# Performance work log

Hardware: AMD Instinct MI355X
Metric: run time of the kernel (lower is better)

The kernel has to match this reference:

```python
import jax, jax.numpy as jnp
import numpy as np

HOP = 256
B, F, NB = 16, 4096, 65

def setup_inputs() -> dict:
    key = jax.random.key(0)
    k1, k2 = jax.random.split(key)
    filter_bank = jax.random.normal(k1, (B, F, NB), dtype=jnp.float32)
    noise_u = jax.random.uniform(k2, (B, F, HOP), dtype=jnp.float32)
    return {"filter_bank": filter_bank, "noise_u": noise_u}

def amp_to_impulse_response(amp, target_size):
    # treat real amp as complex spectrum with zero imag, go to time domain
    amp_c = jax.lax.complex(amp, jnp.zeros_like(amp))
    ir = jnp.fft.irfft(amp_c, axis=-1)            # [B, F, 2*(NB-1)]
    filter_size = ir.shape[-1]
    ir = jnp.roll(ir, filter_size // 2, axis=-1)
    n = jnp.arange(filter_size, dtype=ir.dtype)
    win = 0.5 * (1.0 - jnp.cos(2.0 * jnp.pi * n / filter_size))  # periodic hann (torch default)
    ir = ir * win
    ir = jnp.pad(ir, ((0, 0), (0, 0), (0, target_size - filter_size)))
    ir = jnp.roll(ir, -(filter_size // 2), axis=-1)
    return ir

def fft_convolve(signal, kernel):
    n = signal.shape[-1]
    sig = jnp.pad(signal, ((0, 0), (0, 0), (0, n)))
    ker = jnp.pad(kernel, ((0, 0), (0, 0), (kernel.shape[-1], 0)))
    out = jnp.fft.irfft(jnp.fft.rfft(sig) * jnp.fft.rfft(ker))
    return out[..., out.shape[-1] // 2:]

def reference(filter_bank, noise_u):
    impulse = amp_to_impulse_response(filter_bank, HOP)   # [B, F, HOP]
    noise = noise_u * 2.0 - 1.0                           # [B, F, HOP]
    out = fft_convolve(noise, impulse)                    # [B, F, HOP]
    return out.reshape(out.shape[0], -1, 1)               # [B, F*HOP, 1]
```

## Files before the change

### kernel.cpp

```cpp
#include <hip/hip_runtime.h>
#include <math.h>

#define NB 65
#define HOPS 256
#define RPB 4
#define THREADS 64
#define TAPS_OFF 360
#define RSTRIDE 492

#define PHYS(i) ((i) + (((i) >> 5) << 2))

#define WAVE_FENCE() do { asm volatile("" ::: "memory"); __builtin_amdgcn_wave_barrier(); } while (0)

__device__ __forceinline__ void load16(float (&d)[16], const float* p) {
#pragma unroll
    for (int x = 0; x < 4; ++x) {
        float4 v = *(const float4*)(p + 4 * x);
        d[4*x] = v.x; d[4*x+1] = v.y; d[4*x+2] = v.z; d[4*x+3] = v.w;
    }
}
__device__ __forceinline__ void load16s(float (&d)[16], const float* rowbuf, int L) {
#pragma unroll
    for (int x = 0; x < 4; ++x) {
        float4 v = *(const float4*)(rowbuf + PHYS(L + 4 * x));
        d[4*x] = v.x; d[4*x+1] = v.y; d[4*x+2] = v.z; d[4*x+3] = v.w;
    }
}
__device__ __forceinline__ void fma16(float (&f)[16], const float (&tp)[16],
                                      const float (&lo)[16], const float (&hi)[16]) {
#pragma unroll
    for (int kk = 0; kk < 16; ++kk) {
        float t = tp[kk];
#pragma unroll
        for (int d = 0; d < 16; ++d) {
            int j = 16 + d - kk;
            f[d] = fmaf(t, (j < 16) ? lo[j] : hi[j - 16], f[d]);
        }
    }
}

__global__ __launch_bounds__(THREADS, 4) void noisefilter_kernel(
    const float* __restrict__ fb,
    const float* __restrict__ nz,
    float* __restrict__ out)
{
    __shared__ float lds[RPB * RSTRIDE];
    const int tid  = threadIdx.x;
    const int lane = tid;
    const int r    = tid >> 4;
    const int l16  = tid & 15;
    const int t0   = l16 << 4;
    const size_t row0 = (size_t)blockIdx.x * RPB;
    float* rowbuf = &lds[r * RSTRIDE];

    {
        const float* fbw = fb + row0 * NB;
        for (int i = lane; i < RPB * NB; i += 64) {
            int rr = i / NB;
            int k  = i - rr * NB;
            lds[rr * RSTRIDE + TAPS_OFF + k] = fbw[i];
        }
    }

    const float4* nz4 = (const float4*)(nz + row0 * HOPS);
    float4 nv[4];
#pragma unroll
    for (int p = 0; p < 4; ++p) nv[p] = nz4[lane + p * 64];

    WAVE_FENCE();

    const float alphaA = (float)l16 * 0.04908738521234052f;
    const float alphaB = alphaA + 0.7853981633974483f;
    const float cA = __cosf(alphaA), cB = __cosf(alphaB);
    const float c2A = fmaf(2.0f * cA, cA, -1.0f);
    const float c2B = fmaf(2.0f * cB, cB, -1.0f);
    const float k2A = c2A + c2A, k2B = c2B + c2B;

    float eA1=0.f,eA2=0.f,oA1=0.f,oA2=0.f;
    float eB1=0.f,eB2=0.f,oB1=0.f,oB2=0.f;
    float s32 = 0.f, a0r = 0.f, a64r;

    const float* amp = rowbuf + TAPS_OFF;
    {
        float a = amp[64];
        a64r = a;
        { float t = a - eA2; float s = fmaf(k2A, eA1, t); eA2 = eA1; eA1 = s; }
        { float t = a - eB2; float s = fmaf(k2B, eB1, t); eB2 = eB1; eB1 = s; }
        s32 += a;
    }
#pragma unroll
    for (int kb = 48; kb >= 0; kb -= 16) {
        float ab[16];
        load16(ab, amp + kb);
#pragma unroll
        for (int kk = 15; kk >= 0; --kk) {
            float a = ab[kk];
            if (kk & 1) {
                { float t = a - oA2; float s = fmaf(k2A, oA1, t); oA2 = oA1; oA1 = s; }
                { float t = a - oB2; float s = fmaf(k2B, oB1, t); oB2 = oB1; oB1 = s; }
            } else {
                { float t = a - eA2; float s = fmaf(k2A, eA1, t); eA2 = eA1; eA1 = s; }
                { float t = a - eB2; float s = fmaf(k2B, eB1, t); eB2 = eB1; eB1 = s; }
                if ((kk >> 1) & 1) s32 -= a; else s32 += a;
            }
        }
        if (kb == 0) a0r = ab[0];
    }

    const float EA = fmaf(-c2A, eA2, eA1);
    const float OA = cA * (oA1 - oA2);
    const float EB = fmaf(-c2B, eB2, eB1);
    const float OB = cB * (oB1 - oB2);
    const float pm = (l16 & 1) ? -1.f : 1.f;
    const float corr = fmaf(pm, a64r, a0r);
    const float inv = 1.0f / 256.0f;
    float* tps = rowbuf + TAPS_OFF;

    {
        float GA  = fmaf(2.f, EA + OA, -corr);
        float GAm = fmaf(2.f, EA - OA, -corr);
        float TA  = GA  * (1.0f + cA) * inv;
        float TAm = GAm * (1.0f - cA) * inv;
        tps[l16] = TA;
        tps[64 - l16] = TAm;
        if (l16 >= 1) { tps[128 - l16] = TA; tps[64 + l16] = TAm; }
    }
    {
        float GB  = fmaf(2.f, EB + OB, -corr);
        float GBm = fmaf(2.f, EB - OB, -corr);
        float TB  = GB  * (1.0f + cB) * inv;
        float TBm = GBm * (1.0f - cB) * inv;
        tps[16 + l16] = TB;  tps[112 - l16] = TB;
        tps[48 - l16] = TBm; tps[80 + l16]  = TBm;
    }
    if (l16 == 0) {
        float G32 = fmaf(2.f, s32, -(a0r + a64r));
        float T32 = G32 * inv;
        tps[32] = T32;
        tps[96] = T32;
    }

    *(float4*)(rowbuf + PHYS(4 * l16)) = make_float4(0.f, 0.f, 0.f, 0.f);

#pragma unroll
    for (int p = 0; p < 4; ++p) {
        float4 v = nv[p];
        int o = (lane << 2) + 64;
        *(float4*)(&lds[p * RSTRIDE + PHYS(o)]) =
            make_float4(fmaf(2.f, v.x, -1.f), fmaf(2.f, v.y, -1.f),
                        fmaf(2.f, v.z, -1.f), fmaf(2.f, v.w, -1.f));
    }

    WAVE_FENCE();

    float f[16];
#pragma unroll
    for (int d = 0; d < 16; ++d) f[d] = 0.f;
    float X[16], Y[16], Z[16], tp[16];
    {
        const int b0 = t0 + 48;
        load16s(X, rowbuf, b0);      load16s(Y, rowbuf, b0 + 16);
        load16(tp, tps + 0);   fma16(f, tp, X, Y);
        load16s(Z, rowbuf, b0 - 16);
        load16(tp, tps + 16);  fma16(f, tp, Z, X);
        load16s(Y, rowbuf, b0 - 32);
        load16(tp, tps + 32);  fma16(f, tp, Y, Z);
        load16s(X, rowbuf, b0 - 48);
        load16(tp, tps + 48);  fma16(f, tp, X, Y);
    }

    float g[4] = {0.f, 0.f, 0.f, 0.f};
#pragma unroll
    for (int c = 0; c < 4; ++c) {
        float W[20];
#pragma unroll
        for (int x = 0; x < 5; ++x) {
            float4 v = *(const float4*)(rowbuf + PHYS(48 + 4 * l16 - 16 * c + 4 * x));
            W[4*x] = v.x; W[4*x+1] = v.y; W[4*x+2] = v.z; W[4*x+3] = v.w;
        }
        float tp2[16];
        load16(tp2, tps + 64 + 16 * c);
#pragma unroll
        for (int kk = 0; kk < 16; ++kk) {
            float t = tp2[kk];
#pragma unroll
            for (int d = 0; d < 4; ++d)
                g[d] = fmaf(t, W[16 + d - kk], g[d]);
        }
    }
    *(float4*)(tps + 64 + 4 * l16) = make_float4(g[0], g[1], g[2], g[3]);
    if (l16 >= 12) {
        const float* sc = tps + 64 + ((l16 - 12) << 4);
#pragma unroll
        for (int x = 0; x < 4; ++x) {
            float4 v = *(const float4*)(sc + 4 * x);
            f[4*x]   += v.x; f[4*x+1] += v.y;
            f[4*x+2] += v.z; f[4*x+3] += v.w;
        }
    }

    float* op = out + (row0 + r) * HOPS + t0;
#pragma unroll
    for (int x = 0; x < 4; ++x)
        *(float4*)(op + 4 * x) = make_float4(f[4*x], f[4*x+1], f[4*x+2], f[4*x+3]);
}

extern "C" void kernel_launch(void* const* d_in, const int* in_sizes, int n_in,
                              void* d_out, int out_size, void* d_ws, size_t ws_size,
                              hipStream_t stream) {
    const float* fb = (const float*)d_in[0];
    const float* nz = (const float*)d_in[1];
    float* o = (float*)d_out;
    const int rows = 16 * 4096;
    noisefilter_kernel<<<dim3(rows / RPB), dim3(THREADS), 0, stream>>>(fb, nz, o);
}
```

Baseline: 151.4 us.

## Process eight rows per wave with 32 outputs per lane

Doubles rows per 64-thread block from 4 to 8, so each lane computes 32 consecutive outputs and four cosine-recurrence frequencies instead of 16 outputs and two. Each loaded window register is reused across more FMAs, which raises arithmetic intensity per LDS read and halves the block count. In exchange it uses more VGPRs (occupancy hint lowered to 2) and halves LDS-limited occupancy, which could expose latency.

```diff
diff --git a/kernel.cpp b/kernel.cpp
--- a/kernel.cpp
+++ b/kernel.cpp
@@ -3,7 +3,7 @@
 
 #define NB 65
 #define HOPS 256
-#define RPB 4
+#define RPB 8
 #define THREADS 64
 #define TAPS_OFF 360
 #define RSTRIDE 492
@@ -26,32 +26,47 @@
         d[4*x] = v.x; d[4*x+1] = v.y; d[4*x+2] = v.z; d[4*x+3] = v.w;
     }
 }
-__device__ __forceinline__ void fma16(float (&f)[16], const float (&tp)[16],
-                                      const float (&lo)[16], const float (&hi)[16]) {
+__device__ __forceinline__ void fma32(float (&f)[32], const float (&tp)[16],
+                                      const float (&b)[16], const float (&m)[16],
+                                      const float (&t)[16]) {
 #pragma unroll
     for (int kk = 0; kk < 16; ++kk) {
-        float t = tp[kk];
-#pragma unroll
-        for (int d = 0; d < 16; ++d) {
+        float tv = tp[kk];
+#pragma unroll
+        for (int d = 0; d < 32; ++d) {
             int j = 16 + d - kk;
-            f[d] = fmaf(t, (j < 16) ? lo[j] : hi[j - 16], f[d]);
-        }
-    }
-}
-
-__global__ __launch_bounds__(THREADS, 4) void noisefilter_kernel(
+            float w = (j < 16) ? b[j] : (j < 32) ? m[j - 16] : t[j - 32];
+            f[d] = fmaf(tv, w, f[d]);
+        }
+    }
+}
+__device__ __forceinline__ void fma8(float (&g)[8], const float (&tp)[16],
+                                     const float (&lo)[16], const float (&hi)[16]) {
+#pragma unroll
+    for (int kk = 0; kk < 16; ++kk) {
+        float tv = tp[kk];
+#pragma unroll
+        for (int d = 0; d < 8; ++d) {
+            int j = 16 + d - kk;
+            float w = (j < 16) ? lo[j] : hi[j - 16];
+            g[d] = fmaf(tv, w, g[d]);
+        }
+    }
+}
+
+__global__ __launch_bounds__(THREADS, 2) void noisefilter_kernel(
     const float* __restrict__ fb,
     const float* __restrict__ nz,
     float* __restrict__ out)
 {
     __shared__ float lds[RPB * RSTRIDE];
-    const int tid  = threadIdx.x;
-    const int lane = tid;
-    const int r    = tid >> 4;
-    const int l16  = tid & 15;
-    const int t0   = l16 << 4;
+    const int lane = threadIdx.x;
+    const int r    = lane >> 3;
+    const int l8   = lane & 7;
+    const int t0   = l8 << 5;
     const size_t row0 = (size_t)blockIdx.x * RPB;
     float* rowbuf = &lds[r * RSTRIDE];
+    float* tps = rowbuf + TAPS_OFF;
 
     {
         const float* fbw = fb + row0 * NB;
@@ -63,31 +78,33 @@
     }
 
     const float4* nz4 = (const float4*)(nz + row0 * HOPS);
-    float4 nv[4];
-#pragma unroll
-    for (int p = 0; p < 4; ++p) nv[p] = nz4[lane + p * 64];
+    float4 nv[8];
+#pragma unroll
+    for (int p = 0; p < 8; ++p) nv[p] = nz4[lane + p * 64];
 
     WAVE_FENCE();
 
-    const float alphaA = (float)l16 * 0.04908738521234052f;
-    const float alphaB = alphaA + 0.7853981633974483f;
-    const float cA = __cosf(alphaA), cB = __cosf(alphaB);
-    const float c2A = fmaf(2.0f * cA, cA, -1.0f);
-    const float c2B = fmaf(2.0f * cB, cB, -1.0f);
-    const float k2A = c2A + c2A, k2B = c2B + c2B;
-
-    float eA1=0.f,eA2=0.f,oA1=0.f,oA2=0.f;
-    float eB1=0.f,eB2=0.f,oB1=0.f,oB2=0.f;
+    float cs[4], c2s[4], k2s[4];
+#pragma unroll
+    for (int m = 0; m < 4; ++m) {
+        float alpha = (float)(l8 + 8 * m) * 0.04908738521234052f;
+        float cm = __cosf(alpha);
+        cs[m] = cm;
+        float c2m = fmaf(2.0f * cm, cm, -1.0f);
+        c2s[m] = c2m;
+        k2s[m] = c2m + c2m;
+    }
+    float e1[4] = {0.f,0.f,0.f,0.f}, e2[4] = {0.f,0.f,0.f,0.f};
+    float o1[4] = {0.f,0.f,0.f,0.f}, o2[4] = {0.f,0.f,0.f,0.f};
     float s32 = 0.f, a0r = 0.f, a64r;
 
-    const float* amp = rowbuf + TAPS_OFF;
-    {
-        float a = amp[64];
-        a64r = a;
-        { float t = a - eA2; float s = fmaf(k2A, eA1, t); eA2 = eA1; eA1 = s; }
-        { float t = a - eB2; float s = fmaf(k2B, eB1, t); eB2 = eB1; eB1 = s; }
-        s32 += a;
-    }
+    const float* amp = tps;
+    a64r = amp[64];
+#pragma unroll
+    for (int m = 0; m < 4; ++m) {
+        float t = a64r - e2[m]; float s = fmaf(k2s[m], e1[m], t); e2[m] = e1[m]; e1[m] = s;
+    }
+    s32 += a64r;
 #pragma unroll
     for (int kb = 48; kb >= 0; kb -= 16) {
         float ab[16];
@@ -96,54 +113,49 @@
         for (int kk = 15; kk >= 0; --kk) {
             float a = ab[kk];
             if (kk & 1) {
-                { float t = a - oA2; float s = fmaf(k2A, oA1, t); oA2 = oA1; oA1 = s; }
-                { float t = a - oB2; float s = fmaf(k2B, oB1, t); oB2 = oB1; oB1 = s; }
+#pragma unroll
+                for (int m = 0; m < 4; ++m) {
+                    float t = a - o2[m]; float s = fmaf(k2s[m], o1[m], t); o2[m] = o1[m]; o1[m] = s;
+                }
             } else {
-                { float t = a - eA2; float s = fmaf(k2A, eA1, t); eA2 = eA1; eA1 = s; }
-                { float t = a - eB2; float s = fmaf(k2B, eB1, t); eB2 = eB1; eB1 = s; }
+#pragma unroll
+                for (int m = 0; m < 4; ++m) {
+                    float t = a - e2[m]; float s = fmaf(k2s[m], e1[m], t); e2[m] = e1[m]; e1[m] = s;
+                }
                 if ((kk >> 1) & 1) s32 -= a; else s32 += a;
             }
         }
         if (kb == 0) a0r = ab[0];
     }
 
-    const float EA = fmaf(-c2A, eA2, eA1);
-    const float OA = cA * (oA1 - oA2);
-    const float EB = fmaf(-c2B, eB2, eB1);
-    const float OB = cB * (oB1 - oB2);
-    const float pm = (l16 & 1) ? -1.f : 1.f;
+    const float pm = (l8 & 1) ? -1.f : 1.f;
     const float corr = fmaf(pm, a64r, a0r);
     const float inv = 1.0f / 256.0f;
-    float* tps = rowbuf + TAPS_OFF;
-
-    {
-        float GA  = fmaf(2.f, EA + OA, -corr);
-        float GAm = fmaf(2.f, EA - OA, -corr);
-        float TA  = GA  * (1.0f + cA) * inv;
-        float TAm = GAm * (1.0f - cA) * inv;
-        tps[l16] = TA;
-        tps[64 - l16] = TAm;
-        if (l16 >= 1) { tps[128 - l16] = TA; tps[64 + l16] = TAm; }
-    }
-    {
-        float GB  = fmaf(2.f, EB + OB, -corr);
-        float GBm = fmaf(2.f, EB - OB, -corr);
-        float TB  = GB  * (1.0f + cB) * inv;
-        float TBm = GBm * (1.0f - cB) * inv;
-        tps[16 + l16] = TB;  tps[112 - l16] = TB;
-        tps[48 - l16] = TBm; tps[80 + l16]  = TBm;
-    }
-    if (l16 == 0) {
+#pragma unroll
+    for (int m = 0; m < 4; ++m) {
+        int n = l8 + 8 * m;
+        float E  = fmaf(-c2s[m], e2[m], e1[m]);
+        float O  = cs[m] * (o1[m] - o2[m]);
+        float G  = fmaf(2.f, E + O, -corr);
+        float Gm = fmaf(2.f, E - O, -corr);
+        float T  = G  * (1.0f + cs[m]) * inv;
+        float Tm = Gm * (1.0f - cs[m]) * inv;
+        tps[n] = T;
+        tps[64 - n] = Tm;
+        if (n >= 1) { tps[128 - n] = T; tps[64 + n] = Tm; }
+    }
+    if (l8 == 0) {
         float G32 = fmaf(2.f, s32, -(a0r + a64r));
         float T32 = G32 * inv;
         tps[32] = T32;
         tps[96] = T32;
     }
 
-    *(float4*)(rowbuf + PHYS(4 * l16)) = make_float4(0.f, 0.f, 0.f, 0.f);
-
-#pragma unroll
-    for (int p = 0; p < 4; ++p) {
+    *(float4*)(rowbuf + PHYS(8 * l8))     = make_float4(0.f, 0.f, 0.f, 0.f);
+    *(float4*)(rowbuf + PHYS(8 * l8 + 4)) = make_float4(0.f, 0.f, 0.f, 0.f);
+
+#pragma unroll
+    for (int p = 0; p < 8; ++p) {
         float4 v = nv[p];
         int o = (lane << 2) + 64;
         *(float4*)(&lds[p * RSTRIDE + PHYS(o)]) =
@@ -153,46 +165,46 @@
 
     WAVE_FENCE();
 
-    float f[16];
-#pragma unroll
-    for (int d = 0; d < 16; ++d) f[d] = 0.f;
-    float X[16], Y[16], Z[16], tp[16];
+    float f[32];
+#pragma unroll
+    for (int d = 0; d < 32; ++d) f[d] = 0.f;
     {
+        float W0[16], W1[16], W2[16], tp[16];
         const int b0 = t0 + 48;
-        load16s(X, rowbuf, b0);      load16s(Y, rowbuf, b0 + 16);
-        load16(tp, tps + 0);   fma16(f, tp, X, Y);
-        load16s(Z, rowbuf, b0 - 16);
-        load16(tp, tps + 16);  fma16(f, tp, Z, X);
-        load16s(Y, rowbuf, b0 - 32);
-        load16(tp, tps + 32);  fma16(f, tp, Y, Z);
-        load16s(X, rowbuf, b0 - 48);
-        load16(tp, tps + 48);  fma16(f, tp, X, Y);
-    }
-
-    float g[4] = {0.f, 0.f, 0.f, 0.f};
-#pragma unroll
-    for (int c = 0; c < 4; ++c) {
-        float W[20];
-#pragma unroll
-        for (int x = 0; x < 5; ++x) {
-            float4 v = *(const float4*)(rowbuf + PHYS(48 + 4 * l16 - 16 * c + 4 * x));
-            W[4*x] = v.x; W[4*x+1] = v.y; W[4*x+2] = v.z; W[4*x+3] = v.w;
-        }
-        float tp2[16];
-        load16(tp2, tps + 64 + 16 * c);
-#pragma unroll
-        for (int kk = 0; kk < 16; ++kk) {
-            float t = tp2[kk];
-#pragma unroll
-            for (int d = 0; d < 4; ++d)
-                g[d] = fmaf(t, W[16 + d - kk], g[d]);
-        }
-    }
-    *(float4*)(tps + 64 + 4 * l16) = make_float4(g[0], g[1], g[2], g[3]);
-    if (l16 >= 12) {
-        const float* sc = tps + 64 + ((l16 - 12) << 4);
-#pragma unroll
-        for (int x = 0; x < 4; ++x) {
+        load16s(W0, rowbuf, b0);
+        load16s(W1, rowbuf, b0 + 16);
+        load16s(W2, rowbuf, b0 + 32);
+        load16(tp, tps + 0);   fma32(f, tp, W0, W1, W2);
+        load16s(W2, rowbuf, b0 - 16);
+        load16(tp, tps + 16);  fma32(f, tp, W2, W0, W1);
+        load16s(W1, rowbuf, b0 - 32);
+        load16(tp, tps + 32);  fma32(f, tp, W1, W2, W0);
+        load16s(W0, rowbuf, b0 - 48);
+        load16(tp, tps + 48);  fma32(f, tp, W0, W1, W2);
+    }
+
+    float g[8];
+#pragma unroll
+    for (int d = 0; d < 8; ++d) g[d] = 0.f;
+    {
+        float V0[16], V1[16], t2[16];
+        const int Bb = 48 + 8 * l8;
+        load16s(V0, rowbuf, Bb);
+        load16s(V1, rowbuf, Bb + 16);
+        load16(t2, tps + 64);   fma8(g, t2, V0, V1);
+        load16s(V1, rowbuf, Bb - 16);
+        load16(t2, tps + 80);   fma8(g, t2, V1, V0);
+        load16s(V0, rowbuf, Bb - 32);
+        load16(t2, tps + 96);   fma8(g, t2, V0, V1);
+        load16s(V1, rowbuf, Bb - 48);
+        load16(t2, tps + 112);  fma8(g, t2, V1, V0);
+    }
+    *(float4*)(tps + 64 + 8 * l8)     = make_float4(g[0], g[1], g[2], g[3]);
+    *(float4*)(tps + 64 + 8 * l8 + 4) = make_float4(g[4], g[5], g[6], g[7]);
+    if (l8 >= 6) {
+        const float* sc = tps + 64 + ((l8 - 6) << 5);
+#pragma unroll
+        for (int x = 0; x < 8; ++x) {
             float4 v = *(const float4*)(sc + 4 * x);
             f[4*x]   += v.x; f[4*x+1] += v.y;
             f[4*x+2] += v.z; f[4*x+3] += v.w;
@@ -201,7 +213,7 @@
 
     float* op = out + (row0 + r) * HOPS + t0;
 #pragma unroll
-    for (int x = 0; x < 4; ++x)
+    for (int x = 0; x < 8; ++x)
         *(float4*)(op + 4 * x) = make_float4(f[4*x], f[4*x+1], f[4*x+2], f[4*x+3]);
 }
 
```

After: 159.2 us. 5.2% more time.
